# Kernel tuning notes

Hardware: AMD Instinct MI355X
Metric: run time of the kernel (lower is better)

The kernel has to match this reference:

```python
import jax, jax.numpy as jnp
import numpy as np

D_MODEL = 1024
D_FF = 4 * D_MODEL
NUM_EXPERTS = 8
TOP_K = 2
B, L = 4, 2048


def setup_inputs() -> dict:
    key = jax.random.key(0)
    ks = jax.random.split(key, 7)
    s = 0.02
    return {
        "x": jax.random.normal(ks[0], (B, L, D_MODEL), dtype=jnp.float32),
        "Wr": jax.random.normal(ks[1], (D_MODEL, NUM_EXPERTS), dtype=jnp.float32) * s,
        "br": jnp.zeros((NUM_EXPERTS,), dtype=jnp.float32),
        "W1": jax.random.normal(ks[2], (NUM_EXPERTS, D_MODEL, D_FF), dtype=jnp.float32) * s,
        "b1": jnp.zeros((NUM_EXPERTS, D_FF), dtype=jnp.float32),
        "W2": jax.random.normal(ks[3], (NUM_EXPERTS, D_FF, D_MODEL), dtype=jnp.float32) * s,
        "b2": jnp.zeros((NUM_EXPERTS, D_MODEL), dtype=jnp.float32),
    }


def reference(x, Wr, br, W1, b1, W2, b2):
    Bb, Ll, D = x.shape
    x_flat = x.reshape(-1, D)                      # [T, D]
    T = x_flat.shape[0]

    # Router: softmax over experts, then top-k and renormalize (matches torch)
    logits = x_flat @ Wr + br                      # [T, E]
    probs = jax.nn.softmax(logits, axis=-1)
    topk_w, topk_idx = jax.lax.top_k(probs, TOP_K)  # [T, K]
    topk_w = topk_w / jnp.sum(topk_w, axis=-1, keepdims=True)

    # Per-token per-expert combine weights: w_full[t, e] = sum_k topk_w[t,k] * (topk_idx[t,k]==e)
    # (top_k indices are distinct, so scatter-add equals the masked-overwrite loop)
    w_full = jnp.zeros((T, NUM_EXPERTS), dtype=x.dtype)
    rows = jnp.arange(T)[:, None]
    w_full = w_full.at[rows, topk_idx].add(topk_w)

    # Dense all-expert MLP (same math as masked per-expert dispatch; dropout is eval/no-op)
    h = jax.nn.gelu(jnp.einsum("td,edf->etf", x_flat, W1) + b1[:, None, :], approximate=False)
    y = jnp.einsum("etf,efd->etd", h, W2) + b2[:, None, :]   # [E, T, D]
    out = jnp.einsum("te,etd->td", w_full, y)                # [T, D]
    return out.reshape(Bb, Ll, D)
```

## Files before the change

### kernel.cpp

```cpp
#include <hip/hip_runtime.h>
#include <hip/hip_bf16.h>

#define T_TOKENS 8192
#define DM 1024
#define DF 4096
#define NE 8
#define NROWS 16384

typedef __attribute__((ext_vector_type(8))) short bf16x8;
typedef __attribute__((ext_vector_type(4))) float f32x4;

__device__ inline unsigned short f2bf(float f) {
  unsigned int u = __builtin_bit_cast(unsigned int, f);
  u = (u + 0x7fffu + ((u >> 16) & 1u)) >> 16;
  return (unsigned short)u;
}

__device__ inline float bf2f(unsigned short s) {
  unsigned int u = ((unsigned int)s) << 16;
  return __builtin_bit_cast(float, u);
}

__device__ __forceinline__ void gload16(const unsigned short* g, unsigned short* l) {
  __builtin_amdgcn_global_load_lds(
      (const __attribute__((address_space(1))) unsigned int*)g,
      (__attribute__((address_space(3))) unsigned int*)l,
      16, 0, 0);
}

__global__ void router_kernel(const float* __restrict__ x,
                              const float* __restrict__ Wr,
                              const float* __restrict__ br,
                              int* __restrict__ ctrl,
                              int* __restrict__ tope,
                              float* __restrict__ topw,
                              unsigned short* __restrict__ xb) {
  const int wid = threadIdx.x >> 6;
  const int lane = threadIdx.x & 63;
  const int t = blockIdx.x * 4 + wid;
  const float* xr = x + (size_t)t * DM;
  unsigned short* xbr = xb + (size_t)t * DM;
  float a[NE];
#pragma unroll
  for (int e = 0; e < NE; ++e) a[e] = 0.f;
#pragma unroll
  for (int it = 0; it < 4; ++it) {
    const int d0 = it * 256 + lane * 4;
    const float4 xv = *(const float4*)(xr + d0);
    ushort4 o;
    o.x = f2bf(xv.x); o.y = f2bf(xv.y); o.z = f2bf(xv.z); o.w = f2bf(xv.w);
    *(ushort4*)(xbr + d0) = o;
    const float xs[4] = {xv.x, xv.y, xv.z, xv.w};
#pragma unroll
    for (int j = 0; j < 4; ++j) {
      const float4 wa = *(const float4*)(Wr + (size_t)(d0 + j) * NE);
      const float4 wb = *(const float4*)(Wr + (size_t)(d0 + j) * NE + 4);
      a[0] += xs[j] * wa.x; a[1] += xs[j] * wa.y;
      a[2] += xs[j] * wa.z; a[3] += xs[j] * wa.w;
      a[4] += xs[j] * wb.x; a[5] += xs[j] * wb.y;
      a[6] += xs[j] * wb.z; a[7] += xs[j] * wb.w;
    }
  }
#pragma unroll
  for (int off = 32; off > 0; off >>= 1) {
#pragma unroll
    for (int e = 0; e < NE; ++e) a[e] += __shfl_xor(a[e], off);
  }
  if (lane == 0) {
    float lg[NE];
    float m = -1e30f;
#pragma unroll
    for (int e = 0; e < NE; ++e) { lg[e] = a[e] + br[e]; m = fmaxf(m, lg[e]); }
    float p[NE];
#pragma unroll
    for (int e = 0; e < NE; ++e) p[e] = expf(lg[e] - m);
    int i0 = 0;
#pragma unroll
    for (int e = 1; e < NE; ++e) if (p[e] > p[i0]) i0 = e;
    int i1 = (i0 == 0) ? 1 : 0;
#pragma unroll
    for (int e = 0; e < NE; ++e) if (e != i0 && p[e] > p[i1]) i1 = e;
    const float s = p[i0] + p[i1];
    tope[2 * t] = i0;
    tope[2 * t + 1] = i1;
    topw[2 * t] = p[i0] / s;
    topw[2 * t + 1] = p[i1] / s;
    atomicAdd(&ctrl[i0], 1);
    atomicAdd(&ctrl[i1], 1);
  }
}

__global__ void scan_kernel(int* __restrict__ ctrl) {
  if (threadIdx.x == 0 && blockIdx.x == 0) {
    int off = 0;
    for (int e = 0; e < NE; ++e) {
      ctrl[8 + e] = off;
      ctrl[20 + e] = off;
      off += ctrl[e];
    }
    ctrl[16] = off;
  }
}

__global__ void place_kernel(const int* __restrict__ tope,
                             const float* __restrict__ topw,
                             int* __restrict__ ctrl,
                             int* __restrict__ rowlist,
                             float* __restrict__ roww,
                             int* __restrict__ posmap) {
  const int t = blockIdx.x * blockDim.x + threadIdx.x;
#pragma unroll
  for (int k = 0; k < 2; ++k) {
    const int e = tope[2 * t + k];
    const int pos = atomicAdd(&ctrl[20 + e], 1);
    rowlist[pos] = t;
    roww[pos] = topw[2 * t + k];
    posmap[2 * t + k] = pos;
  }
}

__global__ void transpose_cvt_kernel(const float* __restrict__ in,
                                     unsigned short* __restrict__ outp,
                                     int R, int C) {
  __shared__ float tile[64][65];
  const int e = blockIdx.z;
  const int r0 = blockIdx.y * 64;
  const int c0 = blockIdx.x * 64;
  const float* src = in + ((size_t)e * R + r0) * C + c0;
#pragma unroll
  for (int i = 0; i < 16; ++i) {
    const int rr = (threadIdx.x >> 6) + i * 4;
    const int cc = threadIdx.x & 63;
    tile[rr][cc] = src[(size_t)rr * C + cc];
  }
  __syncthreads();
  unsigned short* dst = outp + ((size_t)e * C + c0) * R + r0;
#pragma unroll
  for (int i = 0; i < 8; ++i) {
    const int rr = (threadIdx.x >> 5) + i * 8;
    const int cc = (threadIdx.x & 31) * 2;
    const unsigned int lo = f2bf(tile[cc][rr]);
    const unsigned int hi = f2bf(tile[cc + 1][rr]);
    *(unsigned int*)(dst + (size_t)rr * R + cc) = lo | (hi << 16);
  }
}

__global__ __launch_bounds__(256, 4) void gemm1_kernel(
    const unsigned short* __restrict__ xb,
    const unsigned short* __restrict__ w1t,
    const float* __restrict__ b1,
    const int* __restrict__ ctrl,
    const int* __restrict__ rowlist,
    unsigned short* __restrict__ h) {
  const int e = blockIdx.z;
  const int count = ctrl[e];
  const int mt = blockIdx.x;
  if (mt * 128 >= count) return;
  const int off = ctrl[8 + e];
  const int n0 = blockIdx.y * 128;
  const int tid = threadIdx.x;
  const int wid = tid >> 6;
  const int lane = tid & 63;
  const int wm = (wid & 1) * 64;
  const int wn = (wid >> 1) * 64;
  const int q = lane >> 4;
  const int l16 = lane & 15;
  const int rl = lane >> 3;
  const int ch = lane & 7;
  const int sch = ch ^ rl;

  __shared__ __attribute__((aligned(16))) unsigned short lA[128 * 64];
  __shared__ __attribute__((aligned(16))) unsigned short lB[128 * 64];

  const unsigned short* aBase[4];
  const unsigned short* bBase[4];
  unsigned short* lABase[4];
  unsigned short* lBBase[4];
#pragma unroll
  for (int i = 0; i < 4; ++i) {
    const int r = wid * 32 + i * 8 + rl;
    int rr = mt * 128 + r;
    if (rr >= count) rr = count - 1;
    const int tok = rowlist[off + rr];
    aBase[i] = xb + (size_t)tok * DM + sch * 8;
    bBase[i] = w1t + ((size_t)e * DF + n0 + r) * DM + sch * 8;
    lABase[i] = &lA[(wid * 32 + i * 8) * 64];
    lBBase[i] = &lB[(wid * 32 + i * 8) * 64];
  }

  f32x4 acc[4][4];
  const f32x4 z = {0.f, 0.f, 0.f, 0.f};
#pragma unroll
  for (int im = 0; im < 4; ++im)
#pragma unroll
    for (int in = 0; in < 4; ++in) acc[im][in] = z;

  for (int k0 = 0; k0 < DM; k0 += 64) {
#pragma unroll
    for (int i = 0; i < 4; ++i) gload16(aBase[i] + k0, lABase[i]);
#pragma unroll
    for (int i = 0; i < 4; ++i) gload16(bBase[i] + k0, lBBase[i]);
    __syncthreads();
#pragma unroll
    for (int ks = 0; ks < 2; ++ks) {
      const int pc = ((ks * 4 + q) ^ (l16 & 7)) * 8;
      bf16x8 af[4], bfr[4];
#pragma unroll
      for (int im = 0; im < 4; ++im)
        af[im] = *(const bf16x8*)&lA[(wm + im * 16 + l16) * 64 + pc];
#pragma unroll
      for (int in = 0; in < 4; ++in)
        bfr[in] = *(const bf16x8*)&lB[(wn + in * 16 + l16) * 64 + pc];
#pragma unroll
      for (int im = 0; im < 4; ++im)
#pragma unroll
        for (int in = 0; in < 4; ++in)
          acc[im][in] = __builtin_amdgcn_mfma_f32_16x16x32_bf16(
              bfr[in], af[im], acc[im][in], 0, 0, 0);
    }
    __syncthreads();
  }

#pragma unroll
  for (int im = 0; im < 4; ++im) {
    const int r = mt * 128 + wm + im * 16 + l16;
    if (r < count) {
      unsigned short* hrow = h + ((size_t)(off + r)) * DF + n0 + wn + q * 4;
#pragma unroll
      for (int in = 0; in < 4; ++in) {
        const float4 bv = *(const float4*)(b1 + (size_t)e * DF + n0 + wn + in * 16 + q * 4);
        float v0 = acc[im][in][0] + bv.x;
        float v1 = acc[im][in][1] + bv.y;
        float v2 = acc[im][in][2] + bv.z;
        float v3 = acc[im][in][3] + bv.w;
        ushort4 o;
        o.x = f2bf(0.5f * v0 * (1.0f + erff(v0 * 0.70710678118f)));
        o.y = f2bf(0.5f * v1 * (1.0f + erff(v1 * 0.70710678118f)));
        o.z = f2bf(0.5f * v2 * (1.0f + erff(v2 * 0.70710678118f)));
        o.w = f2bf(0.5f * v3 * (1.0f + erff(v3 * 0.70710678118f)));
        *(ushort4*)(hrow + in * 16) = o;
      }
    }
  }
}

__global__ __launch_bounds__(256, 2) void gemm2_kernel(
    const unsigned short* __restrict__ h,
    const unsigned short* __restrict__ w2t,
    const float* __restrict__ b2,
    const int* __restrict__ ctrl,
    unsigned short* __restrict__ y) {
  const int e = blockIdx.z;
  const int count = ctrl[e];
  const int mt = blockIdx.x;
  if (mt * 128 >= count) return;
  const int off = ctrl[8 + e];
  const int n0 = blockIdx.y * 256;
  const int tid = threadIdx.x;
  const int wid = tid >> 6;
  const int lane = tid & 63;
  const int wm = (wid & 1) * 64;
  const int wn = (wid >> 1) * 128;
  const int q = lane >> 4;
  const int l16 = lane & 15;
  const int rl = lane >> 3;
  const int ch = lane & 7;
  const int sch = ch ^ rl;

  __shared__ __attribute__((aligned(16))) unsigned short lA[128 * 64];
  __shared__ __attribute__((aligned(16))) unsigned short lB[256 * 64];

  const unsigned short* aBase[4];
  const unsigned short* bBase[8];
  unsigned short* lABase[4];
  unsigned short* lBBase[8];
#pragma unroll
  for (int i = 0; i < 4; ++i) {
    const int r = wid * 32 + i * 8 + rl;
    int rr = mt * 128 + r;
    if (rr >= count) rr = count - 1;
    aBase[i] = h + (size_t)(off + rr) * DF + sch * 8;
    lABase[i] = &lA[(wid * 32 + i * 8) * 64];
  }
#pragma unroll
  for (int i = 0; i < 8; ++i) {
    const int r = wid * 64 + i * 8 + rl;
    bBase[i] = w2t + ((size_t)e * DM + n0 + r) * DF + sch * 8;
    lBBase[i] = &lB[(wid * 64 + i * 8) * 64];
  }

  f32x4 acc[4][8];
  const f32x4 z = {0.f, 0.f, 0.f, 0.f};
#pragma unroll
  for (int im = 0; im < 4; ++im)
#pragma unroll
    for (int in = 0; in < 8; ++in) acc[im][in] = z;

  for (int k0 = 0; k0 < DF; k0 += 64) {
#pragma unroll
    for (int i = 0; i < 4; ++i) gload16(aBase[i] + k0, lABase[i]);
#pragma unroll
    for (int i = 0; i < 8; ++i) gload16(bBase[i] + k0, lBBase[i]);
    __syncthreads();
#pragma unroll
    for (int ks = 0; ks < 2; ++ks) {
      const int pc = ((ks * 4 + q) ^ (l16 & 7)) * 8;
      bf16x8 af[4], bfr[8];
#pragma unroll
      for (int im = 0; im < 4; ++im)
        af[im] = *(const bf16x8*)&lA[(wm + im * 16 + l16) * 64 + pc];
#pragma unroll
      for (int in = 0; in < 8; ++in)
        bfr[in] = *(const bf16x8*)&lB[(wn + in * 16 + l16) * 64 + pc];
#pragma unroll
      for (int im = 0; im < 4; ++im)
#pragma unroll
        for (int in = 0; in < 8; ++in)
          acc[im][in] = __builtin_amdgcn_mfma_f32_16x16x32_bf16(
              bfr[in], af[im], acc[im][in], 0, 0, 0);
    }
    __syncthreads();
  }

#pragma unroll
  for (int im = 0; im < 4; ++im) {
    const int r = mt * 128 + wm + im * 16 + l16;
    if (r < count) {
      unsigned short* yrow = y + ((size_t)(off + r)) * DM + n0 + wn + q * 4;
#pragma unroll
      for (int in = 0; in < 8; ++in) {
        const float4 bv = *(const float4*)(b2 + (size_t)e * DM + n0 + wn + in * 16 + q * 4);
        ushort4 o;
        o.x = f2bf(acc[im][in][0] + bv.x);
        o.y = f2bf(acc[im][in][1] + bv.y);
        o.z = f2bf(acc[im][in][2] + bv.z);
        o.w = f2bf(acc[im][in][3] + bv.w);
        *(ushort4*)(yrow + in * 16) = o;
      }
    }
  }
}

__global__ void combine_kernel(const unsigned short* __restrict__ y,
                               const int* __restrict__ posmap,
                               const float* __restrict__ topw,
                               float* __restrict__ out) {
  const int t = blockIdx.x;
  const int c = threadIdx.x * 4;
  const int p0 = posmap[2 * t];
  const int p1 = posmap[2 * t + 1];
  const float w0 = topw[2 * t];
  const float w1 = topw[2 * t + 1];
  const ushort4 a = *(const ushort4*)(y + (size_t)p0 * DM + c);
  const ushort4 b = *(const ushort4*)(y + (size_t)p1 * DM + c);
  float4 o;
  o.x = w0 * bf2f(a.x) + w1 * bf2f(b.x);
  o.y = w0 * bf2f(a.y) + w1 * bf2f(b.y);
  o.z = w0 * bf2f(a.z) + w1 * bf2f(b.z);
  o.w = w0 * bf2f(a.w) + w1 * bf2f(b.w);
  *(float4*)(out + (size_t)t * DM + c) = o;
}

extern "C" void kernel_launch(void* const* d_in, const int* in_sizes, int n_in,
                              void* d_out, int out_size, void* d_ws, size_t ws_size,
                              hipStream_t stream) {
  const float* x  = (const float*)d_in[0];
  const float* Wr = (const float*)d_in[1];
  const float* br = (const float*)d_in[2];
  const float* W1 = (const float*)d_in[3];
  const float* b1 = (const float*)d_in[4];
  const float* W2 = (const float*)d_in[5];
  const float* b2 = (const float*)d_in[6];
  float* out = (float*)d_out;

  char* p = (char*)d_ws;
  auto alloc = [&](size_t bytes) -> char* {
    char* r = p;
    p += (bytes + 255) & ~(size_t)255;
    return r;
  };
  int* ctrl = (int*)alloc(1024);
  int* tope = (int*)alloc((size_t)2 * T_TOKENS * 4);
  float* topw = (float*)alloc((size_t)2 * T_TOKENS * 4);
  int* rowlist = (int*)alloc((size_t)NROWS * 4);
  float* roww = (float*)alloc((size_t)NROWS * 4);
  int* posmap = (int*)alloc((size_t)NROWS * 4);
  unsigned short* xb  = (unsigned short*)alloc((size_t)T_TOKENS * DM * 2);
  unsigned short* w1t = (unsigned short*)alloc((size_t)NE * DF * DM * 2);
  unsigned short* w2t = (unsigned short*)alloc((size_t)NE * DM * DF * 2);
  unsigned short* h   = (unsigned short*)alloc((size_t)NROWS * DF * 2);
  if ((size_t)(p - (char*)d_ws) > ws_size) return;

  unsigned short* y = w1t;

  hipMemsetAsync(ctrl, 0, 1024, stream);

  router_kernel<<<T_TOKENS / 4, 256, 0, stream>>>(x, Wr, br, ctrl, tope, topw, xb);
  scan_kernel<<<1, 64, 0, stream>>>(ctrl);
  place_kernel<<<T_TOKENS / 256, 256, 0, stream>>>(tope, topw, ctrl, rowlist, roww, posmap);
  transpose_cvt_kernel<<<dim3(DF / 64, DM / 64, NE), 256, 0, stream>>>(W1, w1t, DM, DF);
  transpose_cvt_kernel<<<dim3(DM / 64, DF / 64, NE), 256, 0, stream>>>(W2, w2t, DF, DM);
  gemm1_kernel<<<dim3(64, DF / 128, NE), 256, 0, stream>>>(xb, w1t, b1, ctrl, rowlist, h);
  gemm2_kernel<<<dim3(64, DM / 256, NE), 256, 0, stream>>>(h, w2t, b2, ctrl, y);
  combine_kernel<<<T_TOKENS, 256, 0, stream>>>(y, posmap, topw, out);
}
```

Measured before the change: 1.254 ms.

## Double-buffer LDS tiles in both expert GEMMs and reorder gemm1 grid

Both grouped GEMM kernels now use two LDS buffers, so the next K tile's global-to-LDS loads are issued before the MFMAs on the current tile run, hiding load latency behind compute. Launch bounds are lowered to match the doubled shared memory. The gemm1 grid is swapped so N tiles vary fastest, meaning consecutive blocks share the same token rows, which should improve L2 reuse of activations. The cost is lower occupancy (half the resident blocks) and the wait on all outstanding loads at each barrier.

```diff
diff --git a/kernel.cpp b/kernel.cpp
--- a/kernel.cpp
+++ b/kernel.cpp
@@ -145,7 +145,7 @@
   }
 }
 
-__global__ __launch_bounds__(256, 4) void gemm1_kernel(
+__global__ __launch_bounds__(256, 2) void gemm1_kernel(
     const unsigned short* __restrict__ xb,
     const unsigned short* __restrict__ w1t,
     const float* __restrict__ b1,
@@ -154,10 +154,10 @@
     unsigned short* __restrict__ h) {
   const int e = blockIdx.z;
   const int count = ctrl[e];
-  const int mt = blockIdx.x;
+  const int mt = blockIdx.y;
   if (mt * 128 >= count) return;
   const int off = ctrl[8 + e];
-  const int n0 = blockIdx.y * 128;
+  const int n0 = blockIdx.x * 128;
   const int tid = threadIdx.x;
   const int wid = tid >> 6;
   const int lane = tid & 63;
@@ -169,13 +169,12 @@
   const int ch = lane & 7;
   const int sch = ch ^ rl;
 
-  __shared__ __attribute__((aligned(16))) unsigned short lA[128 * 64];
-  __shared__ __attribute__((aligned(16))) unsigned short lB[128 * 64];
+  __shared__ __attribute__((aligned(16))) unsigned short lA[2][128 * 64];
+  __shared__ __attribute__((aligned(16))) unsigned short lB[2][128 * 64];
 
   const unsigned short* aBase[4];
   const unsigned short* bBase[4];
-  unsigned short* lABase[4];
-  unsigned short* lBBase[4];
+  int slab[4];
 #pragma unroll
   for (int i = 0; i < 4; ++i) {
     const int r = wid * 32 + i * 8 + rl;
@@ -184,8 +183,7 @@
     const int tok = rowlist[off + rr];
     aBase[i] = xb + (size_t)tok * DM + sch * 8;
     bBase[i] = w1t + ((size_t)e * DF + n0 + r) * DM + sch * 8;
-    lABase[i] = &lA[(wid * 32 + i * 8) * 64];
-    lBBase[i] = &lB[(wid * 32 + i * 8) * 64];
+    slab[i] = (wid * 32 + i * 8) * 64;
   }
 
   f32x4 acc[4][4];
@@ -195,22 +193,32 @@
 #pragma unroll
     for (int in = 0; in < 4; ++in) acc[im][in] = z;
 
-  for (int k0 = 0; k0 < DM; k0 += 64) {
-#pragma unroll
-    for (int i = 0; i < 4; ++i) gload16(aBase[i] + k0, lABase[i]);
-#pragma unroll
-    for (int i = 0; i < 4; ++i) gload16(bBase[i] + k0, lBBase[i]);
-    __syncthreads();
+  const int NT = DM / 64;
+#pragma unroll
+  for (int i = 0; i < 4; ++i) gload16(aBase[i], &lA[0][slab[i]]);
+#pragma unroll
+  for (int i = 0; i < 4; ++i) gload16(bBase[i], &lB[0][slab[i]]);
+  asm volatile("s_waitcnt vmcnt(0)" ::: "memory");
+  __builtin_amdgcn_s_barrier();
+
+  for (int kt = 0; kt + 1 < NT; ++kt) {
+    const int cur = kt & 1;
+    const int nxt = cur ^ 1;
+    const int knext = (kt + 1) * 64;
+#pragma unroll
+    for (int i = 0; i < 4; ++i) gload16(aBase[i] + knext, &lA[nxt][slab[i]]);
+#pragma unroll
+    for (int i = 0; i < 4; ++i) gload16(bBase[i] + knext, &lB[nxt][slab[i]]);
 #pragma unroll
     for (int ks = 0; ks < 2; ++ks) {
       const int pc = ((ks * 4 + q) ^ (l16 & 7)) * 8;
       bf16x8 af[4], bfr[4];
 #pragma unroll
       for (int im = 0; im < 4; ++im)
-        af[im] = *(const bf16x8*)&lA[(wm + im * 16 + l16) * 64 + pc];
+        af[im] = *(const bf16x8*)&lA[cur][(wm + im * 16 + l16) * 64 + pc];
 #pragma unroll
       for (int in = 0; in < 4; ++in)
-        bfr[in] = *(const bf16x8*)&lB[(wn + in * 16 + l16) * 64 + pc];
+        bfr[in] = *(const bf16x8*)&lB[cur][(wn + in * 16 + l16) * 64 + pc];
 #pragma unroll
       for (int im = 0; im < 4; ++im)
 #pragma unroll
@@ -218,7 +226,28 @@
           acc[im][in] = __builtin_amdgcn_mfma_f32_16x16x32_bf16(
               bfr[in], af[im], acc[im][in], 0, 0, 0);
     }
-    __syncthreads();
+    asm volatile("s_waitcnt vmcnt(0)" ::: "memory");
+    __builtin_amdgcn_s_barrier();
+  }
+  {
+    const int cur = (NT - 1) & 1;
+#pragma unroll
+    for (int ks = 0; ks < 2; ++ks) {
+      const int pc = ((ks * 4 + q) ^ (l16 & 7)) * 8;
+      bf16x8 af[4], bfr[4];
+#pragma unroll
+      for (int im = 0; im < 4; ++im)
+        af[im] = *(const bf16x8*)&lA[cur][(wm + im * 16 + l16) * 64 + pc];
+#pragma unroll
+      for (int in = 0; in < 4; ++in)
+        bfr[in] = *(const bf16x8*)&lB[cur][(wn + in * 16 + l16) * 64 + pc];
+#pragma unroll
+      for (int im = 0; im < 4; ++im)
+#pragma unroll
+        for (int in = 0; in < 4; ++in)
+          acc[im][in] = __builtin_amdgcn_mfma_f32_16x16x32_bf16(
+              bfr[in], af[im], acc[im][in], 0, 0, 0);
+    }
   }
 
 #pragma unroll
@@ -244,7 +273,7 @@
   }
 }
 
-__global__ __launch_bounds__(256, 2) void gemm2_kernel(
+__global__ __launch_bounds__(256, 1) void gemm2_kernel(
     const unsigned short* __restrict__ h,
     const unsigned short* __restrict__ w2t,
     const float* __restrict__ b2,
@@ -267,26 +296,25 @@
   const int ch = lane & 7;
   const int sch = ch ^ rl;
 
-  __shared__ __attribute__((aligned(16))) unsigned short lA[128 * 64];
-  __shared__ __attribute__((aligned(16))) unsigned short lB[256 * 64];
+  __shared__ __attribute__((aligned(16))) unsigned short lA[2][128 * 64];
+  __shared__ __attribute__((aligned(16))) unsigned short lB[2][256 * 64];
 
   const unsigned short* aBase[4];
   const unsigned short* bBase[8];
-  unsigned short* lABase[4];
-  unsigned short* lBBase[8];
+  int aSlab[4], bSlab[8];
 #pragma unroll
   for (int i = 0; i < 4; ++i) {
     const int r = wid * 32 + i * 8 + rl;
     int rr = mt * 128 + r;
     if (rr >= count) rr = count - 1;
     aBase[i] = h + (size_t)(off + rr) * DF + sch * 8;
-    lABase[i] = &lA[(wid * 32 + i * 8) * 64];
+    aSlab[i] = (wid * 32 + i * 8) * 64;
   }
 #pragma unroll
   for (int i = 0; i < 8; ++i) {
     const int r = wid * 64 + i * 8 + rl;
     bBase[i] = w2t + ((size_t)e * DM + n0 + r) * DF + sch * 8;
-    lBBase[i] = &lB[(wid * 64 + i * 8) * 64];
+    bSlab[i] = (wid * 64 + i * 8) * 64;
   }
 
   f32x4 acc[4][8];
@@ -296,22 +324,32 @@
 #pragma unroll
     for (int in = 0; in < 8; ++in) acc[im][in] = z;
 
-  for (int k0 = 0; k0 < DF; k0 += 64) {
-#pragma unroll
-    for (int i = 0; i < 4; ++i) gload16(aBase[i] + k0, lABase[i]);
-#pragma unroll
-    for (int i = 0; i < 8; ++i) gload16(bBase[i] + k0, lBBase[i]);
-    __syncthreads();
+  const int NT = DF / 64;
+#pragma unroll
+  for (int i = 0; i < 4; ++i) gload16(aBase[i], &lA[0][aSlab[i]]);
+#pragma unroll
+  for (int i = 0; i < 8; ++i) gload16(bBase[i], &lB[0][bSlab[i]]);
+  asm volatile("s_waitcnt vmcnt(0)" ::: "memory");
+  __builtin_amdgcn_s_barrier();
+
+  for (int kt = 0; kt + 1 < NT; ++kt) {
+    const int cur = kt & 1;
+    const int nxt = cur ^ 1;
+    const int knext = (kt + 1) * 64;
+#pragma unroll
+    for (int i = 0; i < 4; ++i) gload16(aBase[i] + knext, &lA[nxt][aSlab[i]]);
+#pragma unroll
+    for (int i = 0; i < 8; ++i) gload16(bBase[i] + knext, &lB[nxt][bSlab[i]]);
 #pragma unroll
     for (int ks = 0; ks < 2; ++ks) {
       const int pc = ((ks * 4 + q) ^ (l16 & 7)) * 8;
       bf16x8 af[4], bfr[8];
 #pragma unroll
       for (int im = 0; im < 4; ++im)
-        af[im] = *(const bf16x8*)&lA[(wm + im * 16 + l16) * 64 + pc];
+        af[im] = *(const bf16x8*)&lA[cur][(wm + im * 16 + l16) * 64 + pc];
 #pragma unroll
       for (int in = 0; in < 8; ++in)
-        bfr[in] = *(const bf16x8*)&lB[(wn + in * 16 + l16) * 64 + pc];
+        bfr[in] = *(const bf16x8*)&lB[cur][(wn + in * 16 + l16) * 64 + pc];
 #pragma unroll
       for (int im = 0; im < 4; ++im)
 #pragma unroll
@@ -319,7 +357,28 @@
           acc[im][in] = __builtin_amdgcn_mfma_f32_16x16x32_bf16(
               bfr[in], af[im], acc[im][in], 0, 0, 0);
     }
-    __syncthreads();
+    asm volatile("s_waitcnt vmcnt(0)" ::: "memory");
+    __builtin_amdgcn_s_barrier();
+  }
+  {
+    const int cur = (NT - 1) & 1;
+#pragma unroll
+    for (int ks = 0; ks < 2; ++ks) {
+      const int pc = ((ks * 4 + q) ^ (l16 & 7)) * 8;
+      bf16x8 af[4], bfr[8];
+#pragma unroll
+      for (int im = 0; im < 4; ++im)
+        af[im] = *(const bf16x8*)&lA[cur][(wm + im * 16 + l16) * 64 + pc];
+#pragma unroll
+      for (int in = 0; in < 8; ++in)
+        bfr[in] = *(const bf16x8*)&lB[cur][(wn + in * 16 + l16) * 64 + pc];
+#pragma unroll
+      for (int im = 0; im < 4; ++im)
+#pragma unroll
+        for (int in = 0; in < 8; ++in)
+          acc[im][in] = __builtin_amdgcn_mfma_f32_16x16x32_bf16(
+              bfr[in], af[im], acc[im][in], 0, 0, 0);
+    }
   }
 
 #pragma unroll
@@ -400,7 +459,7 @@
   place_kernel<<<T_TOKENS / 256, 256, 0, stream>>>(tope, topw, ctrl, rowlist, roww, posmap);
   transpose_cvt_kernel<<<dim3(DF / 64, DM / 64, NE), 256, 0, stream>>>(W1, w1t, DM, DF);
   transpose_cvt_kernel<<<dim3(DM / 64, DF / 64, NE), 256, 0, stream>>>(W2, w2t, DF, DM);
-  gemm1_kernel<<<dim3(64, DF / 128, NE), 256, 0, stream>>>(xb, w1t, b1, ctrl, rowlist, h);
+  gemm1_kernel<<<dim3(DF / 128, 64, NE), 256, 0, stream>>>(xb, w1t, b1, ctrl, rowlist, h);
   gemm2_kernel<<<dim3(64, DM / 256, NE), 256, 0, stream>>>(h, w2t, b2, ctrl, y);
   combine_kernel<<<T_TOKENS, 256, 0, stream>>>(y, posmap, topw, out);
 }
```

New measurement: 1.492 ms. +18.9%, slower.
